# Kernel tuning notes

Measured on AMD Instinct MI355X. Metric: run time of the kernel, lower is better.

## Reference

```python
import jax, jax.numpy as jnp
import numpy as np

B, T, V, D, H, DK = 64, 384, 12, 256, 4, 64

def _ln(x, g, b):
    m = jnp.mean(x, -1, keepdims=True)
    v = jnp.var(x, -1, keepdims=True)
    return (x - m) * jax.lax.rsqrt(v + 1e-5) * g + b

def _grn(x, W1, b1, W2, b2, Wg, bg, lng, lnb, ctx=None, Wc=None, Ws=None, bs=None):
    # eta2 = ELU(fc1(x) + ctx_proj(ctx)); eta1 = fc2(eta2); GLU; residual; LN
    h = x @ W1 + b1
    if ctx is not None:
        h = h + ctx @ Wc
    h = jax.nn.elu(h)
    h = h @ W2 + b2
    g = h @ Wg + bg
    a, gate = jnp.split(g, 2, axis=-1)
    gated = a * jax.nn.sigmoid(gate)
    skip = x if Ws is None else x @ Ws + bs
    return _ln(skip + gated, lng, lnb)

def setup_inputs() -> dict:
    key = jax.random.key(0)
    ks = iter(jax.random.split(key, 48))
    def rn(shape, s=0.02):
        return jax.random.normal(next(ks), shape, jnp.float32) * s
    return {
        'x': jax.random.normal(next(ks), (B, T, V, D), jnp.float32),
        'context': jax.random.normal(next(ks), (B, D), jnp.float32),
        # flattened GRN of VSN: in=V*D, hidden=D, out=V, context=D, skip needed
        'fg_W1': rn((V * D, D)), 'fg_b1': jnp.zeros((D,), jnp.float32),
        'fg_Wc': rn((D, D)),
        'fg_W2': rn((D, D)), 'fg_b2': jnp.zeros((D,), jnp.float32),
        'fg_Wg': rn((D, 2 * V)), 'fg_bg': jnp.zeros((2 * V,), jnp.float32),
        'fg_Ws': rn((V * D, V)), 'fg_bs': jnp.zeros((V,), jnp.float32),
        'fg_lng': jnp.ones((V,), jnp.float32), 'fg_lnb': jnp.zeros((V,), jnp.float32),
        # per-variable GRNs (V of them, in=out=hidden=D, no skip/ctx), stacked
        'sv_W1': rn((V, D, D)), 'sv_b1': jnp.zeros((V, D), jnp.float32),
        'sv_W2': rn((V, D, D)), 'sv_b2': jnp.zeros((V, D), jnp.float32),
        'sv_Wg': rn((V, D, 2 * D)), 'sv_bg': jnp.zeros((V, 2 * D), jnp.float32),
        'sv_lng': jnp.ones((V, D), jnp.float32), 'sv_lnb': jnp.zeros((V, D), jnp.float32),
        # static enrichment GRN: in=out=hidden=D with context
        'en_W1': rn((D, D)), 'en_b1': jnp.zeros((D,), jnp.float32),
        'en_Wc': rn((D, D)),
        'en_W2': rn((D, D)), 'en_b2': jnp.zeros((D,), jnp.float32),
        'en_Wg': rn((D, 2 * D)), 'en_bg': jnp.zeros((2 * D,), jnp.float32),
        'en_lng': jnp.ones((D,), jnp.float32), 'en_lnb': jnp.zeros((D,), jnp.float32),
        # interpretable MHA: per-head Q/K, shared V, output proj
        'Wq': rn((H, D, DK)), 'Wk': rn((H, D, DK)),
        'Wv': rn((D, DK)), 'Wo': rn((DK, D)),
    }

def reference(x, context, fg_W1, fg_b1, fg_Wc, fg_W2, fg_b2, fg_Wg, fg_bg, fg_Ws, fg_bs,
              fg_lng, fg_lnb, sv_W1, sv_b1, sv_W2, sv_b2, sv_Wg, sv_bg, sv_lng, sv_lnb,
              en_W1, en_b1, en_Wc, en_W2, en_b2, en_Wg, en_bg, en_lng, en_lnb,
              Wq, Wk, Wv, Wo):
    b, t, v, d = x.shape
    ctx3 = context[:, None, :]  # broadcast static context over time
    # ---- Variable Selection Network ----
    xf = x.reshape(b, t, v * d)
    w = _grn(xf, fg_W1, fg_b1, fg_W2, fg_b2, fg_Wg, fg_bg, fg_lng, fg_lnb,
             ctx=ctx3, Wc=fg_Wc, Ws=fg_Ws, bs=fg_bs)
    w = jax.nn.softmax(w, axis=-1)  # (b,t,v)
    per_var = jax.vmap(_grn, in_axes=(2, 0, 0, 0, 0, 0, 0, 0, 0), out_axes=2)(
        x, sv_W1, sv_b1, sv_W2, sv_b2, sv_Wg, sv_bg, sv_lng, sv_lnb)  # (b,t,v,d)
    sel = jnp.sum(per_var * w[..., None], axis=2)  # (b,t,d)
    # ---- static enrichment GRN ----
    enr = _grn(sel, en_W1, en_b1, en_W2, en_b2, en_Wg, en_bg, en_lng, en_lnb,
               ctx=ctx3, Wc=en_Wc)
    # ---- interpretable multi-head attention (causal), per-head Q/K, shared V ----
    q = jnp.einsum('btd,hdk->hbtk', enr, Wq)
    k = jnp.einsum('btd,hdk->hbtk', enr, Wk)
    vp = enr @ Wv  # (b,t,dk), shared across heads
    scale = jax.lax.rsqrt(jnp.asarray(DK, jnp.float32))
    scores = jnp.einsum('hbqd,hbkd->hbqk', q, k) * scale
    mask = jnp.triu(jnp.ones((t, t), bool), 1)  # True = masked (future)
    scores = jnp.where(mask, jnp.asarray(-1e9, scores.dtype), scores)
    attn = jax.nn.softmax(scores, axis=-1)
    heads = jnp.einsum('hbqk,bkd->hbqd', attn, vp)
    out = jnp.mean(heads, axis=0) @ Wo  # mean over heads then shared output proj
    return out
```

## Files before the change

kernel.cpp:

```cpp
#include <hip/hip_runtime.h>
#include <hip/hip_bf16.h>
#include <stdint.h>
#include <stddef.h>

typedef __bf16 bf16;
typedef __bf16 bf16x8 __attribute__((ext_vector_type(8)));
typedef float  f32x4  __attribute__((ext_vector_type(4)));

#define BTR 24576
#define EPI_BIAS  1
#define EPI_CVEC  2
#define EPI_ELU   4
#define EPI_ATTN  8
#define EPI_GATE  32
#define EPI_PERM  64

typedef const __attribute__((address_space(1))) void gas_void;
typedef __attribute__((address_space(3))) void sas_void;
__device__ __forceinline__ void gload16(const void* g, void* s) {
  __builtin_amdgcn_global_load_lds((gas_void*)g, (sas_void*)s, 16, 0, 0);
}
template<int N> __device__ __forceinline__ void waitvm() {
  asm volatile("s_waitcnt vmcnt(%0)" :: "n"(N) : "memory");
}

__device__ __forceinline__ int perm512(int n) {
  return (n < 256) ? (((n >> 4) << 5) + (n & 15))
                   : ((((n - 256) >> 4) << 5) + ((n - 256) & 15) + 16);
}

template<int EPI, bool AF32, bool CF32, int KT = 0>
__global__ __launch_bounds__(256, 2)
void gemm_kernel(const void* __restrict__ Av, int lda, long sAh, long sAb,
                 const bf16* __restrict__ Bt, int ldb, long sBh, long sBb,
                 void* __restrict__ Cv, int ldc, long sC,
                 int K, int zdiv,
                 const float* __restrict__ bias, const float* __restrict__ cvec,
                 long sBias)
{
  constexpr int NBUF = (KT > 0) ? (KT / 32) : 2;
  __shared__ __align__(16) bf16 As[NBUF][128 * 32];
  __shared__ __align__(16) bf16 Bs[NBUF][128 * 32];

  const int tid  = threadIdx.x;
  const int wave = tid >> 6, lane = tid & 63;
  const int wr = wave >> 1, wc = wave & 1;
  const int quad = lane >> 4, l16 = lane & 15;

  const int z  = blockIdx.z;
  const int hh = z / zdiv, bb = z % zdiv;
  const float* AbF = nullptr; const bf16* AbH = nullptr;
  if constexpr (AF32) AbF = (const float*)Av + (long)hh * sAh + (long)bb * sAb;
  else                AbH = (const bf16*)Av  + (long)hh * sAh + (long)bb * sAb;
  const bf16* Bb = Bt + (long)hh * sBh + (long)bb * sBb;
  float* CbF = nullptr; bf16* CbH = nullptr;
  if constexpr (CF32) CbF = (float*)Cv + (long)z * sC;
  else                CbH = (bf16*)Cv  + (long)z * sC;

  const int rowBase = blockIdx.y * 128;
  const int colBase = blockIdx.x * 128;

  f32x4 acc[4][4];
#pragma unroll
  for (int i = 0; i < 4; ++i)
#pragma unroll
    for (int j = 0; j < 4; ++j) { acc[i][j][0]=0.f; acc[i][j][1]=0.f; acc[i][j][2]=0.f; acc[i][j][3]=0.f; }

  const int r0 = tid >> 2, kc = tid & 3;
  const int r1 = tid >> 1, kh = (tid & 1) * 16;
  const int arow = (wr * 64 + l16) * 32 + quad * 8;
  const int brow = (wc * 64 + l16) * 32 + quad * 8;

  if constexpr (KT > 0) {
    constexpr int NT = KT / 32;
    char* AsB = (char*)&As[0][0] + wave * 1024;
    char* BsB = (char*)&Bs[0][0] + wave * 1024;
#pragma unroll
    for (int t = 0; t < NT; ++t) {
      const int k0 = t * 32;
      gload16(AbH + (size_t)(rowBase + r0)      * lda + k0 + kc * 8, AsB + t * 8192);
      gload16(AbH + (size_t)(rowBase + 64 + r0) * lda + k0 + kc * 8, AsB + t * 8192 + 4096);
      gload16(Bb  + (size_t)(colBase + r0)      * ldb + k0 + kc * 8, BsB + t * 8192);
      gload16(Bb  + (size_t)(colBase + 64 + r0) * ldb + k0 + kc * 8, BsB + t * 8192 + 4096);
    }
#define FP_TILE(T)                                                                 \
    if constexpr ((T) < NT) {                                                      \
      waitvm<(NT - 1 - (T)) * 4>();                                                \
      __builtin_amdgcn_s_barrier();                                                \
      const bf16* Asc = &As[(T)][0];                                               \
      const bf16* Bsc = &Bs[(T)][0];                                               \
      bf16x8 af[4], bfv[4];                                                        \
      _Pragma("unroll")                                                            \
      for (int mi = 0; mi < 4; ++mi) af[mi]  = *(const bf16x8*)(Asc + arow + mi * 512); \
      _Pragma("unroll")                                                            \
      for (int ni = 0; ni < 4; ++ni) bfv[ni] = *(const bf16x8*)(Bsc + brow + ni * 512); \
      _Pragma("unroll")                                                            \
      for (int mi = 0; mi < 4; ++mi)                                               \
        _Pragma("unroll")                                                          \
        for (int ni = 0; ni < 4; ++ni)                                             \
          acc[mi][ni] = __builtin_amdgcn_mfma_f32_16x16x32_bf16(af[mi], bfv[ni], acc[mi][ni], 0, 0, 0); \
    }
    FP_TILE(0) FP_TILE(1) FP_TILE(2) FP_TILE(3)
    FP_TILE(4) FP_TILE(5) FP_TILE(6) FP_TILE(7)
#undef FP_TILE
  } else {
    char* AsW = (char*)&As[0][0] + wave * 1024;
    char* BsW = (char*)&Bs[0][0] + wave * 1024;
    f32x4 pf0, pf1, pf2, pf3;
    const int nt = K >> 5;
    int cur = 0;

    if constexpr (AF32) {
      const float* p = AbF + (size_t)(rowBase + r1) * lda + kh;
      pf0 = *(const f32x4*)(p);     pf1 = *(const f32x4*)(p + 4);
      pf2 = *(const f32x4*)(p + 8); pf3 = *(const f32x4*)(p + 12);
    } else {
      gload16(AbH + (size_t)(rowBase + r0)      * lda + kc * 8, AsW);
      gload16(AbH + (size_t)(rowBase + 64 + r0) * lda + kc * 8, AsW + 4096);
    }
    gload16(Bb + (size_t)(colBase + r0)      * ldb + kc * 8, BsW);
    gload16(Bb + (size_t)(colBase + 64 + r0) * ldb + kc * 8, BsW + 4096);
    if constexpr (AF32) {
      bf16x8 a0, a1;
#pragma unroll
      for (int e = 0; e < 4; ++e) {
        a0[e] = (bf16)pf0[e]; a0[4 + e] = (bf16)pf1[e];
        a1[e] = (bf16)pf2[e]; a1[4 + e] = (bf16)pf3[e];
      }
      *(bf16x8*)(&As[0][0] + r1 * 32 + kh)     = a0;
      *(bf16x8*)(&As[0][0] + r1 * 32 + kh + 8) = a1;
    }
    __syncthreads();

    for (int t = 0; t < nt; ++t) {
      const int nxt = cur ^ 1;
      if (t + 1 < nt) {
        const int k1 = (t + 1) * 32;
        if constexpr (AF32) {
          const float* p = AbF + (size_t)(rowBase + r1) * lda + k1 + kh;
          pf0 = *(const f32x4*)(p);     pf1 = *(const f32x4*)(p + 4);
          pf2 = *(const f32x4*)(p + 8); pf3 = *(const f32x4*)(p + 12);
        } else {
          gload16(AbH + (size_t)(rowBase + r0)      * lda + k1 + kc * 8, AsW + nxt * 8192);
          gload16(AbH + (size_t)(rowBase + 64 + r0) * lda + k1 + kc * 8, AsW + nxt * 8192 + 4096);
        }
        gload16(Bb + (size_t)(colBase + r0)      * ldb + k1 + kc * 8, BsW + nxt * 8192);
        gload16(Bb + (size_t)(colBase + 64 + r0) * ldb + k1 + kc * 8, BsW + nxt * 8192 + 4096);
      }

      const bf16* Asc = &As[cur][0];
      const bf16* Bsc = &Bs[cur][0];
      bf16x8 af[4], bfv[4];
#pragma unroll
      for (int mi = 0; mi < 4; ++mi) af[mi]  = *(const bf16x8*)(Asc + arow + mi * 512);
#pragma unroll
      for (int ni = 0; ni < 4; ++ni) bfv[ni] = *(const bf16x8*)(Bsc + brow + ni * 512);
#pragma unroll
      for (int mi = 0; mi < 4; ++mi)
#pragma unroll
        for (int ni = 0; ni < 4; ++ni)
          acc[mi][ni] = __builtin_amdgcn_mfma_f32_16x16x32_bf16(af[mi], bfv[ni], acc[mi][ni], 0, 0, 0);

      if constexpr (AF32) {
        if (t + 1 < nt) {
          bf16x8 a0, a1;
#pragma unroll
          for (int e = 0; e < 4; ++e) {
            a0[e] = (bf16)pf0[e]; a0[4 + e] = (bf16)pf1[e];
            a1[e] = (bf16)pf2[e]; a1[4 + e] = (bf16)pf3[e];
          }
          *(bf16x8*)(&As[nxt][0] + r1 * 32 + kh)     = a0;
          *(bf16x8*)(&As[nxt][0] + r1 * 32 + kh + 8) = a1;
        }
      }
      __syncthreads();
      cur = nxt;
    }
  }

  if constexpr (EPI & EPI_GATE) {
    const float* bp = bias + (size_t)z * sBias;
#pragma unroll
    for (int mi = 0; mi < 4; ++mi) {
#pragma unroll
      for (int nj = 0; nj < 2; ++nj) {
        const int ni = nj * 2;
        const int pa = colBase + wc * 64 + ni * 16 + l16;
        const int j  = (colBase >> 1) + wc * 32 + nj * 16 + l16;
        const float ba = bp[pa], bg = bp[pa + 16];
        const int row0 = rowBase + wr * 64 + mi * 16 + quad * 4;
#pragma unroll
        for (int r = 0; r < 4; ++r) {
          float a = acc[mi][ni][r]     + ba;
          float g = acc[mi][ni + 1][r] + bg;
          CbH[(size_t)(row0 + r) * ldc + j] = (bf16)(a / (1.f + __expf(-g)));
        }
      }
    }
    return;
  }
  const int bctx = (EPI & EPI_CVEC) ? (rowBase / 384) : 0;
  const float* bp = (EPI & EPI_BIAS) ? bias + (size_t)z * sBias : nullptr;
#pragma unroll
  for (int mi = 0; mi < 4; ++mi) {
#pragma unroll
    for (int ni = 0; ni < 4; ++ni) {
      const int row0 = rowBase + wr * 64 + mi * 16 + quad * 4;
      const int col  = colBase + wc * 64 + ni * 16 + l16;
      float bv = (EPI & EPI_BIAS) ? bp[col] : 0.f;
      float cv = (EPI & EPI_CVEC) ? cvec[bctx * 256 + col] : 0.f;
#pragma unroll
      for (int r = 0; r < 4; ++r) {
        float v = acc[mi][ni][r] + bv + cv;
        if (EPI & EPI_ELU)  v = v > 0.f ? v : __expf(v) - 1.f;
        if (EPI & EPI_ATTN) { v *= 0.125f; if (col > row0 + r) v = -1e9f; }
        int srow = row0 + r;
        if constexpr (EPI & EPI_PERM) srow = perm512(srow);
        if constexpr (CF32) CbF[(size_t)srow * ldc + col] = v;
        else                CbH[(size_t)srow * ldc + col] = (bf16)v;
      }
    }
  }
}

__global__ __launch_bounds__(256, 2)
void fgwide_kernel(const float* __restrict__ A, const bf16* __restrict__ Bt,
                   bf16* __restrict__ C, const float* __restrict__ bias,
                   const float* __restrict__ cvec)
{
  __shared__ __align__(16) bf16 As[2][64 * 32];
  __shared__ __align__(16) bf16 Bs[2][384 * 32];
  const int tid = threadIdx.x;
  const int wave = tid >> 6, lane = tid & 63;
  const int quad = lane >> 4, l16 = lane & 15;
  const int rowBase = blockIdx.x * 64;

  f32x4 acc[4][6];
#pragma unroll
  for (int i = 0; i < 4; ++i)
#pragma unroll
    for (int j = 0; j < 6; ++j) { acc[i][j][0]=0.f; acc[i][j][1]=0.f; acc[i][j][2]=0.f; acc[i][j][3]=0.f; }

  const int r1 = tid >> 2, kh = (tid & 3) * 8;
  const int arow = l16 * 32 + quad * 8;
  const int brow = (wave * 96 + l16) * 32 + quad * 8;

  char* BsW = (char*)&Bs[0][0] + wave * 1024;

  f32x4 pf0, pf1;
  int cur = 0;

  {
    const float* p = A + (size_t)(rowBase + r1) * 3072 + kh;
    pf0 = *(const f32x4*)(p); pf1 = *(const f32x4*)(p + 4);
#pragma unroll
    for (int c = 0; c < 6; ++c) {
      const int idx = c * 256 + tid, rb = idx >> 2, kc2 = idx & 3;
      gload16(Bt + (size_t)rb * 3072 + kc2 * 8, BsW + c * 4096);
    }
    bf16x8 av;
#pragma unroll
    for (int e = 0; e < 4; ++e) { av[e] = (bf16)pf0[e]; av[4 + e] = (bf16)pf1[e]; }
    *(bf16x8*)(&As[0][0] + r1 * 32 + kh) = av;
  }
  __syncthreads();

  for (int t = 0; t < 96; ++t) {
    const int nxt = cur ^ 1;
    if (t + 1 < 96) {
      const int k1 = (t + 1) * 32;
      const float* p = A + (size_t)(rowBase + r1) * 3072 + k1 + kh;
      pf0 = *(const f32x4*)(p); pf1 = *(const f32x4*)(p + 4);
#pragma unroll
      for (int c = 0; c < 6; ++c) {
        const int idx = c * 256 + tid, rb = idx >> 2, kc2 = idx & 3;
        gload16(Bt + (size_t)rb * 3072 + k1 + kc2 * 8, BsW + nxt * 24576 + c * 4096);
      }
    }

    const bf16* Asc = &As[cur][0];
    const bf16* Bsc = &Bs[cur][0];
    bf16x8 af[4], bfv[6];
#pragma unroll
    for (int mi = 0; mi < 4; ++mi) af[mi]  = *(const bf16x8*)(Asc + arow + mi * 512);
#pragma unroll
    for (int ni = 0; ni < 6; ++ni) bfv[ni] = *(const bf16x8*)(Bsc + brow + ni * 512);
#pragma unroll
    for (int mi = 0; mi < 4; ++mi)
#pragma unroll
      for (int ni = 0; ni < 6; ++ni)
        acc[mi][ni] = __builtin_amdgcn_mfma_f32_16x16x32_bf16(af[mi], bfv[ni], acc[mi][ni], 0, 0, 0);

    if (t + 1 < 96) {
      bf16x8 av;
#pragma unroll
      for (int e = 0; e < 4; ++e) { av[e] = (bf16)pf0[e]; av[4 + e] = (bf16)pf1[e]; }
      *(bf16x8*)(&As[nxt][0] + r1 * 32 + kh) = av;
    }
    __syncthreads();
    cur = nxt;
  }

  const int bctx = rowBase / 384;
#pragma unroll
  for (int mi = 0; mi < 4; ++mi) {
#pragma unroll
    for (int ni = 0; ni < 6; ++ni) {
      const int col = wave * 96 + ni * 16 + l16;
      const bool act = (wave * 96 + ni * 16) < 256;
      const float bv = bias[col];
      const float cv = act ? cvec[bctx * 256 + col] : 0.f;
      const int row0 = rowBase + mi * 16 + quad * 4;
#pragma unroll
      for (int r = 0; r < 4; ++r) {
        float v = acc[mi][ni][r] + bv + cv;
        if (act) v = v > 0.f ? v : __expf(v) - 1.f;
        C[(size_t)(row0 + r) * 384 + col] = (bf16)v;
      }
    }
  }
}

__global__ void prep_kernel(
    const float* fgW1, const float* fgWs, const float* fgW2, const float* fgWg,
    const float* fgb1, const float* fgbs,
    const float* svW1, const float* svWg, const float* svW2,
    const float* enW1, const float* enWg, const float* enW2,
    const float* Wq, const float* Wk, const float* Wv, const float* Wo,
    bf16* fgW1WsT, bf16* fgWgPT, bf16* fgW2C, float* bias384,
    bf16* svW1T, bf16* svWgT, bf16* svW2C,
    bf16* enW1T, bf16* enWgT, bf16* enW2C,
    bf16* WqkvT, bf16* WoT)
{
  long i = (long)blockIdx.x * 256 + threadIdx.x;
  if (i < 1179648) {
    int n = i / 3072, k = i % 3072; float v;
    if (n < 256) v = fgW1[(size_t)k * 256 + n];
    else { int nn = n - 256; v = (nn < 12) ? fgWs[(size_t)k * 12 + nn] : 0.f; }
    fgW1WsT[i] = (bf16)v; return; } i -= 1179648;
  if (i < 32768)  { int n = i >> 8, k = i & 255; fgWgPT[i] = (n < 24) ? (bf16)fgWg[k * 24 + n] : (bf16)0.f; return; } i -= 32768;
  if (i < 65536)  { fgW2C[i] = (bf16)fgW2[i]; return; } i -= 65536;
  if (i < 384)    { bias384[i] = (i < 256) ? fgb1[i] : ((i < 268) ? fgbs[i - 256] : 0.f); return; } i -= 384;
  if (i < 786432) { long v = i >> 16, r = i & 65535; int n = r >> 8, k = r & 255; svW1T[i] = (bf16)svW1[(v << 16) + k * 256 + n]; return; } i -= 786432;
  if (i < 1572864){ long v = i >> 17, r = i & 131071; int n = r >> 8, k = r & 255; svWgT[i] = (bf16)svWg[(v << 17) + k * 512 + n]; return; } i -= 1572864;
  if (i < 786432) { svW2C[i] = (bf16)svW2[i]; return; } i -= 786432;
  if (i < 65536)  { int n = i >> 8, k = i & 255; enW1T[i] = (bf16)enW1[k * 256 + n]; return; } i -= 65536;
  if (i < 131072) { int n = i >> 8, k = i & 255; enWgT[i] = (bf16)enWg[k * 512 + n]; return; } i -= 131072;
  if (i < 65536)  { enW2C[i] = (bf16)enW2[i]; return; } i -= 65536;
  if (i < 163840) { int n = i >> 8, k = i & 255; float val;
                    if (n < 256)      val = Wq[(n >> 6) * 16384 + k * 64 + (n & 63)];
                    else if (n < 512) { int nn = n - 256; val = Wk[(nn >> 6) * 16384 + k * 64 + (nn & 63)]; }
                    else if (n < 576) val = Wv[k * 64 + (n - 512)];
                    else              val = 0.f;
                    WqkvT[i] = (bf16)val; return; } i -= 163840;
  if (i < 16384)  { int n = i >> 6, k = i & 63; WoT[i] = (bf16)Wo[k * 256 + n]; }
}

__global__ void biasfuse_kernel(const float* fgb2, const float* fgWg, const float* fgbg,
                                const float* svb2, const float* svWg, const float* svbg,
                                const float* enb2, const float* enWg, const float* enbg,
                                float* fgBF, float* svBFP, float* enBFP)
{
  int i = blockIdx.x * 256 + threadIdx.x;
  if (i < 128) {
    float s = 0.f;
    if (i < 24) { s = fgbg[i]; for (int k = 0; k < 256; ++k) s += fgb2[k] * fgWg[k * 24 + i]; }
    fgBF[i] = s; return; } i -= 128;
  if (i < 6144) {
    int v = i >> 9, n = i & 511;
    float s = svbg[v * 512 + n];
    const float* W = svWg + (size_t)v * 131072;
    const float* b2 = svb2 + v * 256;
    for (int k = 0; k < 256; ++k) s += b2[k] * W[k * 512 + n];
    svBFP[v * 512 + perm512(n)] = s; return; } i -= 6144;
  if (i < 512) {
    float s = enbg[i];
    for (int k = 0; k < 256; ++k) s += enb2[k] * enWg[k * 512 + i];
    enBFP[perm512(i)] = s; }
}

__global__ void cvec_kernel(const float* __restrict__ ctx, const float* __restrict__ WcFg,
                            const float* __restrict__ WcEn, float* __restrict__ outFg,
                            float* __restrict__ outEn) {
  int b = blockIdx.x, n = threadIdx.x;
  const float* Wc = blockIdx.y ? WcEn : WcFg;
  float* o = blockIdx.y ? outEn : outFg;
  float acc = 0.f;
  for (int d = 0; d < 256; ++d) acc += ctx[b * 256 + d] * Wc[d * 256 + n];
  o[b * 256 + n] = acc;
}

__global__ void lnsm12_kernel(const bf16* __restrict__ B384, const bf16* __restrict__ GP,
                              const float* __restrict__ lng, const float* __restrict__ lnb,
                              float* __restrict__ w) {
  int r = blockIdx.x * 256 + threadIdx.x;
  if (r >= BTR) return;
  float y[12]; float m = 0.f;
#pragma unroll
  for (int j = 0; j < 12; ++j) {
    float a = (float)GP[(size_t)r * 128 + j];
    float g = (float)GP[(size_t)r * 128 + 12 + j];
    float gated = a / (1.f + __expf(-g));
    y[j] = (float)B384[(size_t)r * 384 + 256 + j] + gated; m += y[j];
  }
  m *= (1.f / 12.f);
  float var = 0.f;
#pragma unroll
  for (int j = 0; j < 12; ++j) { float d = y[j] - m; var += d * d; }
  var *= (1.f / 12.f);
  float rstd = rsqrtf(var + 1e-5f);
  float mx = -1e30f;
#pragma unroll
  for (int j = 0; j < 12; ++j) { y[j] = (y[j] - m) * rstd * lng[j] + lnb[j]; mx = fmaxf(mx, y[j]); }
  float s = 0.f;
#pragma unroll
  for (int j = 0; j < 12; ++j) { y[j] = __expf(y[j] - mx); s += y[j]; }
  float inv = 1.f / s;
#pragma unroll
  for (int j = 0; j < 12; ++j) w[r * 12 + j] = y[j] * inv;
}

__device__ __forceinline__ void block_sum2(float a, float b, float& oa, float& ob) {
#pragma unroll
  for (int o = 32; o; o >>= 1) { a += __shfl_xor(a, o); b += __shfl_xor(b, o); }
  __shared__ float ra[4], rb[4];
  int w = threadIdx.x >> 6;
  if ((threadIdx.x & 63) == 0) { ra[w] = a; rb[w] = b; }
  __syncthreads();
  oa = ra[0] + ra[1] + ra[2] + ra[3];
  ob = rb[0] + rb[1] + rb[2] + rb[3];
  __syncthreads();
}

__global__ __launch_bounds__(256)
void selacc4_kernel(const bf16* __restrict__ GATED, const float* __restrict__ x,
                    const float* __restrict__ w, const float* __restrict__ lng,
                    const float* __restrict__ lnb, float* __restrict__ sel,
                    bf16* __restrict__ selb, int v0, int isFirst, int isLast) {
  int r = blockIdx.x, d = threadIdx.x;
  float acc = isFirst ? 0.f : sel[(size_t)r * 256 + d];
#pragma unroll
  for (int vv = 0; vv < 4; ++vv) {
    int v = v0 + vv;
    float gated = (float)GATED[(size_t)vv * ((size_t)BTR * 256) + (size_t)r * 256 + d];
    float y = x[(size_t)r * 3072 + v * 256 + d] + gated;
    float s1, s2;
    block_sum2(y, y * y, s1, s2);
    float mean = s1 * (1.f / 256.f);
    float var  = s2 * (1.f / 256.f) - mean * mean;
    float val  = (y - mean) * rsqrtf(var + 1e-5f) * lng[v * 256 + d] + lnb[v * 256 + d];
    acc += w[r * 12 + v] * val;
  }
  if (isLast) selb[(size_t)r * 256 + d] = (bf16)acc;
  else        sel[(size_t)r * 256 + d] = acc;
}

__global__ __launch_bounds__(256)
void enrln_kernel(const bf16* __restrict__ GATED, const bf16* __restrict__ skip,
                  const float* __restrict__ lng, const float* __restrict__ lnb,
                  bf16* __restrict__ out) {
  int r = blockIdx.x, d = threadIdx.x;
  float gated = (float)GATED[(size_t)r * 256 + d];
  float y = (float)skip[(size_t)r * 256 + d] + gated;
  float s1, s2;
  block_sum2(y, y * y, s1, s2);
  float mean = s1 * (1.f / 256.f);
  float var = s2 * (1.f / 256.f) - mean * mean;
  float norm = (y - mean) * rsqrtf(var + 1e-5f);
  out[(size_t)r * 256 + d] = (bf16)(norm * lng[d] + lnb[d]);
}

__global__ __launch_bounds__(256)
void softmax_avg_kernel(const bf16* __restrict__ S, bf16* __restrict__ P) {
  const int wv = threadIdx.x >> 6, lane = threadIdx.x & 63;
  const int bq = blockIdx.x * 4 + wv;
  const int b = bq / 384, q = bq % 384;
  float pb[6];
#pragma unroll
  for (int e = 0; e < 6; ++e) pb[e] = 0.f;
  for (int h = 0; h < 4; ++h) {
    const bf16* row = S + ((size_t)((h * 64 + b) * 384 + q)) * 384;
    float v[6]; float m = -1e30f;
#pragma unroll
    for (int e = 0; e < 6; ++e) { v[e] = (float)row[lane + e * 64]; m = fmaxf(m, v[e]); }
#pragma unroll
    for (int o = 32; o; o >>= 1) m = fmaxf(m, __shfl_xor(m, o));
    float l = 0.f;
#pragma unroll
    for (int e = 0; e < 6; ++e) { v[e] = __expf(v[e] - m); l += v[e]; }
#pragma unroll
    for (int o = 32; o; o >>= 1) l += __shfl_xor(l, o);
    float inv = 1.f / l;
#pragma unroll
    for (int e = 0; e < 6; ++e) pb[e] += v[e] * inv;
  }
  bf16* out = P + (size_t)bq * 384;
#pragma unroll
  for (int e = 0; e < 6; ++e) out[lane + e * 64] = (bf16)(0.25f * pb[e]);
}

template<int EPI, bool AF32, bool CF32, int KT = 0>
static inline void rungemm(hipStream_t s,
    const void* A, int lda, const bf16* Bt, int ldb, void* C, int ldc,
    int M, int N, int K,
    const float* bias = nullptr, const float* cvec = nullptr,
    int Z = 1, int zdiv = 1,
    long sAh = 0, long sAb = 0, long sBh = 0, long sBb = 0, long sC = 0, long sBias = 0)
{
  dim3 grid(N / 128, M / 128, Z);
  gemm_kernel<EPI, AF32, CF32, KT><<<grid, 256, 0, s>>>(A, lda, sAh, sAb, Bt, ldb, sBh, sBb, C, ldc, sC, K, zdiv, bias, cvec, sBias);
}

extern "C" void kernel_launch(void* const* d_in, const int* in_sizes, int n_in,
                              void* d_out, int out_size, void* d_ws, size_t ws_size,
                              hipStream_t stream)
{
  (void)in_sizes; (void)n_in; (void)out_size;
  const float* x      = (const float*)d_in[0];
  const float* ctx    = (const float*)d_in[1];
  const float* fg_W1  = (const float*)d_in[2];
  const float* fg_b1  = (const float*)d_in[3];
  const float* fg_Wc  = (const float*)d_in[4];
  const float* fg_W2  = (const float*)d_in[5];
  const float* fg_b2  = (const float*)d_in[6];
  const float* fg_Wg  = (const float*)d_in[7];
  const float* fg_bg  = (const float*)d_in[8];
  const float* fg_Ws  = (const float*)d_in[9];
  const float* fg_bs  = (const float*)d_in[10];
  const float* fg_lng = (const float*)d_in[11];
  const float* fg_lnb = (const float*)d_in[12];
  const float* sv_W1  = (const float*)d_in[13];
  const float* sv_b1  = (const float*)d_in[14];
  const float* sv_W2  = (const float*)d_in[15];
  const float* sv_b2  = (const float*)d_in[16];
  const float* sv_Wg  = (const float*)d_in[17];
  const float* sv_bg  = (const float*)d_in[18];
  const float* sv_lng = (const float*)d_in[19];
  const float* sv_lnb = (const float*)d_in[20];
  const float* en_W1  = (const float*)d_in[21];
  const float* en_b1  = (const float*)d_in[22];
  const float* en_Wc  = (const float*)d_in[23];
  const float* en_W2  = (const float*)d_in[24];
  const float* en_b2  = (const float*)d_in[25];
  const float* en_Wg  = (const float*)d_in[26];
  const float* en_bg  = (const float*)d_in[27];
  const float* en_lng = (const float*)d_in[28];
  const float* en_lnb = (const float*)d_in[29];
  const float* Wq     = (const float*)d_in[30];
  const float* Wk     = (const float*)d_in[31];
  const float* Wv     = (const float*)d_in[32];
  const float* Wo     = (const float*)d_in[33];

  static constexpr size_t OFF_FGW1WST = 0;
  static constexpr size_t OFF_FGWGPT  = OFF_FGW1WST + 2359296;
  static constexpr size_t OFF_FGW2C   = OFF_FGWGPT  + 65536;
  static constexpr size_t OFF_FGW2GT  = OFF_FGW2C   + 131072;
  static constexpr size_t OFF_BIAS384 = OFF_FGW2GT  + 65536;
  static constexpr size_t OFF_FGBF    = OFF_BIAS384 + 1536;
  static constexpr size_t OFF_SVW1T   = OFF_FGBF    + 512;
  static constexpr size_t OFF_SVWGT   = OFF_SVW1T   + 1572864;
  static constexpr size_t OFF_SVW2C   = OFF_SVWGT   + 3145728;
  static constexpr size_t OFF_SVW2GPT = OFF_SVW2C   + 1572864;
  static constexpr size_t OFF_SVBFP   = OFF_SVW2GPT + 3145728;
  static constexpr size_t OFF_ENW1T   = OFF_SVBFP   + 24576;
  static constexpr size_t OFF_ENWGT   = OFF_ENW1T   + 131072;
  static constexpr size_t OFF_ENW2C   = OFF_ENWGT   + 262144;
  static constexpr size_t OFF_ENW2GPT = OFF_ENW2C   + 131072;
  static constexpr size_t OFF_ENBFP   = OFF_ENW2GPT + 262144;
  static constexpr size_t OFF_WQKVT   = OFF_ENBFP   + 2048;
  static constexpr size_t OFF_WOT     = OFF_WQKVT   + 327680;
  static constexpr size_t OFF_CVECFG  = OFF_WOT     + 32768;
  static constexpr size_t OFF_CVECEN  = OFF_CVECFG  + 65536;
  static constexpr size_t ARENA       = OFF_CVECEN  + 65536;
  static constexpr size_t WS_NEEDED = ARENA + 152174592;

  if (ws_size < WS_NEEDED) return;

  char* ws = (char*)d_ws;
  bf16*  fgW1WsT = (bf16*)(ws + OFF_FGW1WST);
  bf16*  fgWgPT  = (bf16*)(ws + OFF_FGWGPT);
  bf16*  fgW2C   = (bf16*)(ws + OFF_FGW2C);
  bf16*  fgW2gT  = (bf16*)(ws + OFF_FGW2GT);
  float* bias384 = (float*)(ws + OFF_BIAS384);
  float* fgBF    = (float*)(ws + OFF_FGBF);
  bf16*  svW1T   = (bf16*)(ws + OFF_SVW1T);
  bf16*  svWgT   = (bf16*)(ws + OFF_SVWGT);
  bf16*  svW2C   = (bf16*)(ws + OFF_SVW2C);
  bf16*  svW2gPT = (bf16*)(ws + OFF_SVW2GPT);
  float* svBFP   = (float*)(ws + OFF_SVBFP);
  bf16*  enW1T   = (bf16*)(ws + OFF_ENW1T);
  bf16*  enWgT   = (bf16*)(ws + OFF_ENWGT);
  bf16*  enW2C   = (bf16*)(ws + OFF_ENW2C);
  bf16*  enW2gPT = (bf16*)(ws + OFF_ENW2GPT);
  float* enBFP   = (float*)(ws + OFF_ENBFP);
  bf16*  WqkvT   = (bf16*)(ws + OFF_WQKVT);
  bf16*  WoT     = (bf16*)(ws + OFF_WOT);
  float* cvecFg  = (float*)(ws + OFF_CVECFG);
  float* cvecEn  = (float*)(ws + OFF_CVECEN);
  char*  ar      = ws + ARENA;
  float* sel     = (float*)(ar + 0);
  bf16*  selb    = (bf16*)(ar + 25165824);
  float* wbuf    = (float*)(ar + 37748736);
  bf16*  H1G     = (bf16*)(ar + 38928384);
  bf16*  BUF384  = (bf16*)(ar + 38928384);
  bf16*  GPAD    = (bf16*)(ar + 57802752);
  bf16*  H1EN    = (bf16*)(ar + 38928384);
  bf16*  GATED   = (bf16*)(ar + 89260032);
  bf16*  GATEDEN = (bf16*)(ar + 89260032);
  bf16*  enr     = (bf16*)(ar + 139591680);
  bf16*  QKV     = (bf16*)(ar + 0);
  bf16*  Pbar    = (bf16*)(ar + 38928384);
  bf16*  Sbuf    = (bf16*)(ar + 64094208);
  bf16*  UT      = (bf16*)(ar + 64094208);
  float* out     = (float*)d_out;

  prep_kernel<<<19010, 256, 0, stream>>>(fg_W1, fg_Ws, fg_W2, fg_Wg, fg_b1, fg_bs,
                                         sv_W1, sv_Wg, sv_W2, en_W1, en_Wg, en_W2,
                                         Wq, Wk, Wv, Wo,
                                         fgW1WsT, fgWgPT, fgW2C, bias384,
                                         svW1T, svWgT, svW2C, enW1T, enWgT, enW2C,
                                         WqkvT, WoT);
  biasfuse_kernel<<<27, 256, 0, stream>>>(fg_b2, fg_Wg, fg_bg, sv_b2, sv_Wg, sv_bg,
                                          en_b2, en_Wg, en_bg, fgBF, svBFP, enBFP);
  cvec_kernel<<<dim3(64, 2), 256, 0, stream>>>(ctx, fg_Wc, en_Wc, cvecFg, cvecEn);

  rungemm<0,        false, false, 256>(stream, fgWgPT, 256, fgW2C, 256, fgW2gT, 256, 128, 256, 256);
  rungemm<EPI_PERM, false, false, 256>(stream, svWgT, 256, svW2C, 256, svW2gPT, 256, 512, 256, 256,
                                       nullptr, nullptr, 12, 12, 0, 131072, 0, 65536, 131072);
  rungemm<EPI_PERM, false, false, 256>(stream, enWgT, 256, enW2C, 256, enW2gPT, 256, 512, 256, 256);

  fgwide_kernel<<<384, 256, 0, stream>>>(x, fgW1WsT, BUF384, bias384, cvecFg);
  rungemm<EPI_BIAS, false, false, 256>(stream, BUF384, 384, fgW2gT, 256, GPAD, 128, BTR, 128, 256, fgBF);
  lnsm12_kernel<<<96, 256, 0, stream>>>(BUF384, GPAD, fg_lng, fg_lnb, wbuf);

  for (int g = 0; g < 3; ++g) {
    rungemm<EPI_BIAS|EPI_ELU, true, false>(
        stream, x + g * 4 * 256, 3072, svW1T + (size_t)g * 4 * 65536, 256, H1G, 256, BTR, 256, 256,
        sv_b1 + g * 4 * 256, nullptr, 4, 4, 0, 256, 0, 65536, (long)BTR * 256, 256);
    rungemm<EPI_BIAS|EPI_GATE, false, false, 256>(
        stream, H1G, 256, svW2gPT + (size_t)g * 4 * 131072, 256, GATED, 256, BTR, 512, 256,
        svBFP + g * 4 * 512, nullptr, 4, 4, 0, (long)BTR * 256, 0, 131072, (long)BTR * 256, 512);
    selacc4_kernel<<<BTR, 256, 0, stream>>>(GATED, x, wbuf, sv_lng, sv_lnb, sel, selb,
                                            g * 4, g == 0, g == 2);
  }

  rungemm<EPI_BIAS|EPI_CVEC|EPI_ELU, false, false, 256>(stream, selb, 256, enW1T, 256, H1EN, 256, BTR, 256, 256, en_b1, cvecEn);
  rungemm<EPI_BIAS|EPI_GATE, false, false, 256>(stream, H1EN, 256, enW2gPT, 256, GATEDEN, 256, BTR, 512, 256, enBFP);
  enrln_kernel<<<BTR, 256, 0, stream>>>(GATEDEN, selb, en_lng, en_lnb, enr);

  rungemm<0, false, false, 256>(stream, enr, 256, WqkvT, 256, QKV, 640, BTR, 640, 256);
  rungemm<EPI_ATTN, false, false, 64>(stream, QKV, 640, QKV + 256, 640, Sbuf, 384, 384, 384, 64,
                                      nullptr, nullptr, 256, 64, 64, 245760L, 64, 245760L, 147456L);
  softmax_avg_kernel<<<6144, 256, 0, stream>>>(Sbuf, Pbar);
  rungemm<0, false, false, 64>(stream, WoT, 64, QKV + 512, 640, UT, 384, 256, 384, 64,
                               nullptr, nullptr, 64, 64, 0, 0, 0, 245760L, 98304L);
  rungemm<0, false, true>(stream, Pbar, 384, UT, 384, out, 256, 384, 256, 384,
                          nullptr, nullptr, 64, 1, 147456L, 0, 98304L, 0, 98304L);
}
```

Measured before the change: 1.369 ms.

## Ring-buffer K256 GEMM, XCD-aware block remap, causal tile skip, tiled weight transpose

For K=256, the GEMM now streams tiles through a 4-slot LDS ring with three loads in flight, where it previously staged all eight K tiles at once. This cuts LDS use, which may raise occupancy. Workgroup indices are remapped so that consecutive tiles land on the same XCD, which should improve L2 locality. Attention-score tiles above the causal diagonal skip the K loop. Weight transposes move from a strided elementwise prep kernel into a coalesced 32x32 LDS-tiled transpose kernel. Each change adds control-flow complexity, and the remap adds integer division per block.

Result: faster. 1.232 ms (-10.0%).

```diff
diff --git a/kernel.cpp b/kernel.cpp
--- a/kernel.cpp
+++ b/kernel.cpp
@@ -38,7 +38,7 @@
                  const float* __restrict__ bias, const float* __restrict__ cvec,
                  long sBias)
 {
-  constexpr int NBUF = (KT > 0) ? (KT / 32) : 2;
+  constexpr int NBUF = (KT == 256) ? 4 : 2;
   __shared__ __align__(16) bf16 As[NBUF][128 * 32];
   __shared__ __align__(16) bf16 Bs[NBUF][128 * 32];
 
@@ -47,7 +47,19 @@
   const int wr = wave >> 1, wc = wave & 1;
   const int quad = lane >> 4, l16 = lane & 15;
 
-  const int z  = blockIdx.z;
+  const int gx = gridDim.x, gxy = gridDim.x * gridDim.y;
+  const int nwg = gxy * gridDim.z;
+  int lin = (blockIdx.z * gridDim.y + blockIdx.y) * gx + blockIdx.x;
+  {
+    const int q8 = nwg >> 3, r8 = nwg & 7;
+    const int xcd = lin & 7, idx = lin >> 3;
+    lin = (xcd < r8) ? xcd * (q8 + 1) + idx
+                     : r8 * (q8 + 1) + (xcd - r8) * q8 + idx;
+  }
+  const int z  = lin / gxy;
+  const int rem = lin - z * gxy;
+  const int by = rem / gx, bx = rem - by * gx;
+
   const int hh = z / zdiv, bb = z % zdiv;
   const float* AbF = nullptr; const bf16* AbH = nullptr;
   if constexpr (AF32) AbF = (const float*)Av + (long)hh * sAh + (long)bb * sAb;
@@ -57,8 +69,8 @@
   if constexpr (CF32) CbF = (float*)Cv + (long)z * sC;
   else                CbH = (bf16*)Cv  + (long)z * sC;
 
-  const int rowBase = blockIdx.y * 128;
-  const int colBase = blockIdx.x * 128;
+  const int rowBase = by * 128;
+  const int colBase = bx * 128;
 
   f32x4 acc[4][4];
 #pragma unroll
@@ -71,12 +83,47 @@
   const int arow = (wr * 64 + l16) * 32 + quad * 8;
   const int brow = (wc * 64 + l16) * 32 + quad * 8;
 
-  if constexpr (KT > 0) {
-    constexpr int NT = KT / 32;
+  const bool skipK = (EPI & EPI_ATTN) && (colBase > rowBase);
+
+  if (!skipK) {
+  if constexpr (KT == 256) {
     char* AsB = (char*)&As[0][0] + wave * 1024;
     char* BsB = (char*)&Bs[0][0] + wave * 1024;
-#pragma unroll
-    for (int t = 0; t < NT; ++t) {
+#define RT_ISSUE(T)                                                                \
+    { const int k0 = (T) * 32; char* ad = AsB + ((T) & 3) * 8192;                  \
+      char* bd = BsB + ((T) & 3) * 8192;                                           \
+      gload16(AbH + (size_t)(rowBase + r0)      * lda + k0 + kc * 8, ad);          \
+      gload16(AbH + (size_t)(rowBase + 64 + r0) * lda + k0 + kc * 8, ad + 4096);   \
+      gload16(Bb  + (size_t)(colBase + r0)      * ldb + k0 + kc * 8, bd);          \
+      gload16(Bb  + (size_t)(colBase + 64 + r0) * ldb + k0 + kc * 8, bd + 4096); }
+    RT_ISSUE(0) RT_ISSUE(1) RT_ISSUE(2)
+#define RT_TILE(T)                                                                 \
+    {                                                                              \
+      waitvm<((T) < 6) ? 8 : (((T) == 6) ? 4 : 0)>();                              \
+      __builtin_amdgcn_s_barrier();                                                \
+      if constexpr ((T) < 5) RT_ISSUE((T) + 3)                                     \
+      const bf16* Asc = &As[(T) & 3][0];                                           \
+      const bf16* Bsc = &Bs[(T) & 3][0];                                           \
+      bf16x8 af[4], bfv[4];                                                        \
+      _Pragma("unroll")                                                            \
+      for (int mi = 0; mi < 4; ++mi) af[mi]  = *(const bf16x8*)(Asc + arow + mi * 512); \
+      _Pragma("unroll")                                                            \
+      for (int ni = 0; ni < 4; ++ni) bfv[ni] = *(const bf16x8*)(Bsc + brow + ni * 512); \
+      _Pragma("unroll")                                                            \
+      for (int mi = 0; mi < 4; ++mi)                                               \
+        _Pragma("unroll")                                                          \
+        for (int ni = 0; ni < 4; ++ni)                                             \
+          acc[mi][ni] = __builtin_amdgcn_mfma_f32_16x16x32_bf16(af[mi], bfv[ni], acc[mi][ni], 0, 0, 0); \
+    }
+    RT_TILE(0) RT_TILE(1) RT_TILE(2) RT_TILE(3)
+    RT_TILE(4) RT_TILE(5) RT_TILE(6) RT_TILE(7)
+#undef RT_TILE
+#undef RT_ISSUE
+  } else if constexpr (KT == 64) {
+    char* AsB = (char*)&As[0][0] + wave * 1024;
+    char* BsB = (char*)&Bs[0][0] + wave * 1024;
+#pragma unroll
+    for (int t = 0; t < 2; ++t) {
       const int k0 = t * 32;
       gload16(AbH + (size_t)(rowBase + r0)      * lda + k0 + kc * 8, AsB + t * 8192);
       gload16(AbH + (size_t)(rowBase + 64 + r0) * lda + k0 + kc * 8, AsB + t * 8192 + 4096);
@@ -84,8 +131,8 @@
       gload16(Bb  + (size_t)(colBase + 64 + r0) * ldb + k0 + kc * 8, BsB + t * 8192 + 4096);
     }
 #define FP_TILE(T)                                                                 \
-    if constexpr ((T) < NT) {                                                      \
-      waitvm<(NT - 1 - (T)) * 4>();                                                \
+    {                                                                              \
+      waitvm<(1 - (T)) * 4>();                                                     \
       __builtin_amdgcn_s_barrier();                                                \
       const bf16* Asc = &As[(T)][0];                                               \
       const bf16* Bsc = &Bs[(T)][0];                                               \
@@ -100,8 +147,7 @@
         for (int ni = 0; ni < 4; ++ni)                                             \
           acc[mi][ni] = __builtin_amdgcn_mfma_f32_16x16x32_bf16(af[mi], bfv[ni], acc[mi][ni], 0, 0, 0); \
     }
-    FP_TILE(0) FP_TILE(1) FP_TILE(2) FP_TILE(3)
-    FP_TILE(4) FP_TILE(5) FP_TILE(6) FP_TILE(7)
+    FP_TILE(0) FP_TILE(1)
 #undef FP_TILE
   } else {
     char* AsW = (char*)&As[0][0] + wave * 1024;
@@ -177,6 +223,7 @@
       cur = nxt;
     }
   }
+  }
 
   if constexpr (EPI & EPI_GATE) {
     const float* bp = bias + (size_t)z * sBias;
@@ -321,39 +368,58 @@
   }
 }
 
+__global__ __launch_bounds__(256)
+void wtrans_kernel(const float* __restrict__ fgW1, const float* __restrict__ fgWs,
+                   const float* __restrict__ svW1, const float* __restrict__ svWg,
+                   const float* __restrict__ enW1, const float* __restrict__ enWg,
+                   const float* __restrict__ Wo,
+                   bf16* __restrict__ fgW1WsT, bf16* __restrict__ svW1T,
+                   bf16* __restrict__ svWgT, bf16* __restrict__ enW1T,
+                   bf16* __restrict__ enWgT, bf16* __restrict__ WoT)
+{
+  __shared__ float tbuf[32][33];
+  int tile = blockIdx.x;
+  const float* src; bf16* dst; int K, Nsrc, tk, tn;
+  if (tile < 768)        { src = fgW1; dst = fgW1WsT; K = 3072; Nsrc = 256; tk = tile % 96; tn = tile / 96; }
+  else if ((tile -= 768) < 384)  { src = fgWs; dst = fgW1WsT + (size_t)256 * 3072; K = 3072; Nsrc = 12;  tk = tile % 96; tn = tile / 96; }
+  else if ((tile -= 384) < 768)  { int v = tile / 64,  r = tile % 64;
+                                   src = svW1 + (size_t)v * 65536;  dst = svW1T + (size_t)v * 65536;  K = 256; Nsrc = 256; tk = r % 8; tn = r / 8; }
+  else if ((tile -= 768) < 1536) { int v = tile / 128, r = tile % 128;
+                                   src = svWg + (size_t)v * 131072; dst = svWgT + (size_t)v * 131072; K = 256; Nsrc = 512; tk = r % 8; tn = r / 8; }
+  else if ((tile -= 1536) < 64)  { src = enW1; dst = enW1T; K = 256; Nsrc = 256; tk = tile % 8; tn = tile / 8; }
+  else if ((tile -= 64) < 128)   { src = enWg; dst = enWgT; K = 256; Nsrc = 512; tk = tile % 8; tn = tile / 8; }
+  else                           { tile -= 128; src = Wo; dst = WoT; K = 64; Nsrc = 256; tk = tile % 2; tn = tile / 2; }
+  const int tx = threadIdx.x & 31, ty = threadIdx.x >> 5;
+  const int k0 = tk * 32, n0 = tn * 32;
+  const int n = n0 + tx;
+#pragma unroll
+  for (int p = 0; p < 4; ++p)
+    tbuf[ty + 8 * p][tx] = (n < Nsrc) ? src[(size_t)(k0 + ty + 8 * p) * Nsrc + n] : 0.f;
+  __syncthreads();
+#pragma unroll
+  for (int p = 0; p < 4; ++p)
+    dst[(size_t)(n0 + ty + 8 * p) * K + k0 + tx] = (bf16)tbuf[tx][ty + 8 * p];
+}
+
 __global__ void prep_kernel(
-    const float* fgW1, const float* fgWs, const float* fgW2, const float* fgWg,
-    const float* fgb1, const float* fgbs,
-    const float* svW1, const float* svWg, const float* svW2,
-    const float* enW1, const float* enWg, const float* enW2,
-    const float* Wq, const float* Wk, const float* Wv, const float* Wo,
-    bf16* fgW1WsT, bf16* fgWgPT, bf16* fgW2C, float* bias384,
-    bf16* svW1T, bf16* svWgT, bf16* svW2C,
-    bf16* enW1T, bf16* enWgT, bf16* enW2C,
-    bf16* WqkvT, bf16* WoT)
+    const float* fgWg, const float* fgb1, const float* fgbs,
+    const float* fgW2, const float* svW2, const float* enW2,
+    const float* Wq, const float* Wk, const float* Wv,
+    bf16* fgWgPT, bf16* fgW2C, float* bias384,
+    bf16* svW2C, bf16* enW2C, bf16* WqkvT)
 {
   long i = (long)blockIdx.x * 256 + threadIdx.x;
-  if (i < 1179648) {
-    int n = i / 3072, k = i % 3072; float v;
-    if (n < 256) v = fgW1[(size_t)k * 256 + n];
-    else { int nn = n - 256; v = (nn < 12) ? fgWs[(size_t)k * 12 + nn] : 0.f; }
-    fgW1WsT[i] = (bf16)v; return; } i -= 1179648;
   if (i < 32768)  { int n = i >> 8, k = i & 255; fgWgPT[i] = (n < 24) ? (bf16)fgWg[k * 24 + n] : (bf16)0.f; return; } i -= 32768;
   if (i < 65536)  { fgW2C[i] = (bf16)fgW2[i]; return; } i -= 65536;
   if (i < 384)    { bias384[i] = (i < 256) ? fgb1[i] : ((i < 268) ? fgbs[i - 256] : 0.f); return; } i -= 384;
-  if (i < 786432) { long v = i >> 16, r = i & 65535; int n = r >> 8, k = r & 255; svW1T[i] = (bf16)svW1[(v << 16) + k * 256 + n]; return; } i -= 786432;
-  if (i < 1572864){ long v = i >> 17, r = i & 131071; int n = r >> 8, k = r & 255; svWgT[i] = (bf16)svWg[(v << 17) + k * 512 + n]; return; } i -= 1572864;
   if (i < 786432) { svW2C[i] = (bf16)svW2[i]; return; } i -= 786432;
-  if (i < 65536)  { int n = i >> 8, k = i & 255; enW1T[i] = (bf16)enW1[k * 256 + n]; return; } i -= 65536;
-  if (i < 131072) { int n = i >> 8, k = i & 255; enWgT[i] = (bf16)enWg[k * 512 + n]; return; } i -= 131072;
   if (i < 65536)  { enW2C[i] = (bf16)enW2[i]; return; } i -= 65536;
   if (i < 163840) { int n = i >> 8, k = i & 255; float val;
                     if (n < 256)      val = Wq[(n >> 6) * 16384 + k * 64 + (n & 63)];
                     else if (n < 512) { int nn = n - 256; val = Wk[(nn >> 6) * 16384 + k * 64 + (nn & 63)]; }
                     else if (n < 576) val = Wv[k * 64 + (n - 512)];
                     else              val = 0.f;
-                    WqkvT[i] = (bf16)val; return; } i -= 163840;
-  if (i < 16384)  { int n = i >> 6, k = i & 63; WoT[i] = (bf16)Wo[k * 256 + n]; }
+                    WqkvT[i] = (bf16)val; }
 }
 
 __global__ void biasfuse_kernel(const float* fgb2, const float* fgWg, const float* fgbg,
@@ -614,12 +680,11 @@
   bf16*  UT      = (bf16*)(ar + 64094208);
   float* out     = (float*)d_out;
 
-  prep_kernel<<<19010, 256, 0, stream>>>(fg_W1, fg_Ws, fg_W2, fg_Wg, fg_b1, fg_bs,
-                                         sv_W1, sv_Wg, sv_W2, en_W1, en_Wg, en_W2,
-                                         Wq, Wk, Wv, Wo,
-                                         fgW1WsT, fgWgPT, fgW2C, bias384,
-                                         svW1T, svWgT, svW2C, enW1T, enWgT, enW2C,
-                                         WqkvT, WoT);
+  wtrans_kernel<<<3664, 256, 0, stream>>>(fg_W1, fg_Ws, sv_W1, sv_Wg, en_W1, en_Wg, Wo,
+                                          fgW1WsT, svW1T, svWgT, enW1T, enWgT, WoT);
+  prep_kernel<<<4354, 256, 0, stream>>>(fg_Wg, fg_b1, fg_bs, fg_W2, sv_W2, en_W2,
+                                        Wq, Wk, Wv,
+                                        fgWgPT, fgW2C, bias384, svW2C, enW2C, WqkvT);
   biasfuse_kernel<<<27, 256, 0, stream>>>(fg_b2, fg_Wg, fg_bg, sv_b2, sv_Wg, sv_bg,
                                           en_b2, en_Wg, en_bg, fgBF, svBFP, enBFP);
   cvec_kernel<<<dim3(64, 2), 256, 0, stream>>>(ctx, fg_Wc, en_Wc, cvecFg, cvecEn);
```
